# Kernel optimization log

Hardware: AMD Instinct MI355X
Metric: run time of the kernel (lower is better)

## Reference

```python
import jax, jax.numpy as jnp
import numpy as np

N_EMBD = 768
N_HEAD = 12
HEAD_DIM = N_EMBD // N_HEAD  # 64


def setup_inputs() -> dict:
    key = jax.random.key(0)
    k1, k2, k3 = jax.random.split(key, 3)
    B, S = 4, 2048
    x = jax.random.normal(k1, (B, S, N_EMBD), dtype=jnp.float32)
    W_attn = jax.random.normal(k2, (N_EMBD, 3 * N_EMBD), dtype=jnp.float32) * 0.02
    b_attn = jax.random.normal(k3, (3 * N_EMBD,), dtype=jnp.float32) * 0.02
    return {"x": x, "W_attn": W_attn, "b_attn": b_attn}


def reference(x, W_attn, b_attn):
    B, S, E = x.shape
    H, D = N_HEAD, HEAD_DIM
    # fused QKV projection (torch Linear: x @ W^T + b; here W_attn stored as [E, 3E])
    qkv = x @ W_attn + b_attn  # [B, S, 3E]
    q, k, v = jnp.split(qkv, 3, axis=-1)
    q = q.reshape(B, S, H, D)
    k = k.reshape(B, S, H, D)
    v = v.reshape(B, S, H, D)
    scale = 1.0 / np.sqrt(D).astype(np.float32)
    scores = jnp.einsum('bqhd,bkhd->bhqk', q, k) * scale  # [B, H, S, S]
    causal = jnp.tril(jnp.ones((S, S), dtype=bool))
    # ReLU attention nonlinearity (no softmax); masked entries -> 0
    att = jnp.where(causal, jnp.maximum(scores, 0.0), 0.0)
    y = jnp.einsum('bhqk,bkhd->bqhd', att, v)  # [B, S, H, D]
    return y.reshape(B, S, E)
```

## Files before the change

### kernel.cpp

```cpp
#include <hip/hip_runtime.h>

typedef __attribute__((ext_vector_type(8))) short short8;
typedef __attribute__((ext_vector_type(4))) short short4v;
typedef __attribute__((ext_vector_type(4))) float floatx4;
typedef __attribute__((ext_vector_type(2))) unsigned int uint2v;

#define S_LEN 2048
#define NH 12
#define HD 64
#define EMB 768
#define E3 2304
#define N_ITEMS 768

__device__ __forceinline__ unsigned short f2bf(float f) {
    unsigned int u = __builtin_bit_cast(unsigned int, f);
    u += 0x7FFFu + ((u >> 16) & 1u);
    return (unsigned short)(u >> 16);
}

__device__ __forceinline__ unsigned int pack2bf(float a, float b) {
#if __has_builtin(__builtin_amdgcn_cvt_pk_bf16_f32)
    typedef __attribute__((ext_vector_type(2))) short short2v;
    short2v r = __builtin_amdgcn_cvt_pk_bf16_f32(a, b);
    return __builtin_bit_cast(unsigned int, r);
#else
    return (unsigned int)f2bf(a) | ((unsigned int)f2bf(b) << 16);
#endif
}

__device__ __forceinline__ void gl_lds16(const void* g, void* l) {
    __builtin_amdgcn_global_load_lds(
        (const __attribute__((address_space(1))) unsigned int*)g,
        (__attribute__((address_space(3))) unsigned int*)l, 16, 0, 0);
}

__global__ __launch_bounds__(256) void conv_fused(const float* __restrict__ x,
                                                  ushort* __restrict__ xb,
                                                  const float* __restrict__ W,
                                                  ushort* __restrict__ Wt,
                                                  int* __restrict__ counter) {
    int tid = threadIdx.x;
    if (blockIdx.x == 0 && tid == 0) *counter = 0;
    if (blockIdx.x < 6144) {
        int i = (blockIdx.x * 256 + tid) * 4;
        float4 f = *(const float4*)(x + i);
        ushort4 o;
        o.x = f2bf(f.x); o.y = f2bf(f.y); o.z = f2bf(f.z); o.w = f2bf(f.w);
        *(ushort4*)(xb + i) = o;
    } else {
        __shared__ float tile[32][33];
        int b2 = blockIdx.x - 6144;
        int n0 = (b2 % 72) * 32, k0 = (b2 / 72) * 32;
        int tx = tid & 31, ty = tid >> 5;
        for (int i = 0; i < 4; i++)
            tile[ty + i * 8][tx] = W[(size_t)(k0 + ty + i * 8) * E3 + n0 + tx];
        __syncthreads();
        for (int i = 0; i < 4; i++)
            Wt[(size_t)(n0 + ty + i * 8) * EMB + k0 + tx] = f2bf(tile[tx][ty + i * 8]);
    }
}

__global__ __launch_bounds__(256) void qkv_gemm(const ushort* __restrict__ Xb,
                                                const ushort* __restrict__ Wt,
                                                const float* __restrict__ bias,
                                                ushort* __restrict__ QKb,
                                                ushort* __restrict__ Vt) {
    __shared__ ushort lds[33792 / 2];
    ushort* Ald = lds;
    ushort* Bld = lds + 128 * 64;
    int tid  = threadIdx.x;
    int wv = tid >> 6, lane = tid & 63;
    int l15 = lane & 15, quad = lane >> 4;
    int r8 = lane >> 3, cc = lane & 7;
    int wm = wv >> 1, wn = wv & 1;
    int m0 = blockIdx.x * 128, n0 = blockIdx.y * 128;

    floatx4 acc[4][4] = {};

    for (int k0 = 0; k0 < EMB; k0 += 64) {
        __syncthreads();
        for (int i = 0; i < 4; i++) {
            int row = wv * 32 + i * 8 + r8;
            int gc  = cc ^ r8;
            gl_lds16(Xb + (size_t)(m0 + row) * EMB + k0 + gc * 8,
                     (char*)Ald + (wv * 32 + i * 8) * 128);
            gl_lds16(Wt + (size_t)(n0 + row) * EMB + k0 + gc * 8,
                     (char*)Bld + (wv * 32 + i * 8) * 128);
        }
        __syncthreads();
        for (int ch = 0; ch < 2; ch++) {
            int sw = ((ch * 4 + quad) ^ (l15 & 7)) * 16;
            short8 af[4], bf[4];
            for (int mi = 0; mi < 4; mi++)
                af[mi] = *(const short8*)((const char*)Ald + (wm * 64 + mi * 16 + l15) * 128 + sw);
            for (int ni = 0; ni < 4; ni++)
                bf[ni] = *(const short8*)((const char*)Bld + (wn * 64 + ni * 16 + l15) * 128 + sw);
            for (int mi = 0; mi < 4; mi++)
                for (int ni = 0; ni < 4; ni++)
                    acc[mi][ni] = __builtin_amdgcn_mfma_f32_16x16x32_bf16(
                        af[mi], bf[ni], acc[mi][ni], 0, 0, 0);
        }
    }

    __syncthreads();
    if (n0 < 1536) {
        float scale = (n0 < 768) ? 0.125f : 1.0f;
        for (int ni = 0; ni < 4; ni++) {
            int nl = wn * 64 + ni * 16 + l15;
            float bv = bias[n0 + nl];
            for (int mi = 0; mi < 4; mi++)
                for (int r = 0; r < 4; r++) {
                    int ml = wm * 64 + mi * 16 + quad * 4 + r;
                    lds[ml * 132 + nl] = f2bf((acc[mi][ni][r] + bv) * scale);
                }
        }
        __syncthreads();
        int row = tid >> 1, half = tid & 1;
        size_t gm = (size_t)(m0 + row);
        for (int i = 0; i < 8; i++) {
            uint4 v = *(const uint4*)&lds[row * 132 + half * 64 + i * 8];
            *(uint4*)&QKb[gm * 1536 + n0 + half * 64 + i * 8] = v;
        }
    } else {
        for (int ni = 0; ni < 4; ni++) {
            int nl = wn * 64 + ni * 16 + l15;
            float bv = bias[n0 + nl];
            for (int mi = 0; mi < 4; mi++) {
                int ml = wm * 64 + mi * 16 + quad * 4;
                ushort4 pk4;
                pk4.x = f2bf(acc[mi][ni][0] + bv);
                pk4.y = f2bf(acc[mi][ni][1] + bv);
                pk4.z = f2bf(acc[mi][ni][2] + bv);
                pk4.w = f2bf(acc[mi][ni][3] + bv);
                *(ushort4*)&lds[nl * 132 + ml] = pk4;
            }
        }
        __syncthreads();
        int row = tid >> 1, half = tid & 1;
        int nn = n0 + row - 1536;
        int h = nn >> 6, d = nn & 63;
        int b = m0 >> 11, s0 = m0 & 2047;
        for (int i = 0; i < 8; i++) {
            uint4 v = *(const uint4*)&lds[row * 132 + half * 64 + i * 8];
            *(uint4*)&Vt[((size_t)(b * NH + h) * 64 + d) * S_LEN + s0 + half * 64 + i * 8] = v;
        }
    }
}

__global__ __launch_bounds__(256) void attn(const ushort* __restrict__ QKb,
                                            const ushort* __restrict__ Vt,
                                            float* __restrict__ out,
                                            int* __restrict__ counter) {
    __shared__ ushort Kld[2][128 * 64];
    __shared__ ushort Vld[2][64 * 128];
    int* slot = (int*)&Kld[0][0];
    int tid = threadIdx.x;
    int w = tid >> 6, lane = tid & 63;
    int l15 = lane & 15, quad = lane >> 4;
    int r8 = lane >> 3, cc = lane & 7;

    while (true) {
        __syncthreads();
        if (tid == 0) *slot = atomicAdd(counter, 1);
        __syncthreads();
        int it = *slot;
        __syncthreads();
        if (it >= N_ITEMS) break;
        int qt = 15 - it / 48;
        int bh = it % 48;
        int bg = bh / NH, h = bh % NH;

        const ushort* Qcol = QKb + (size_t)bg * S_LEN * 1536 + h * 64;
        const ushort* Kcol = QKb + (size_t)bg * S_LEN * 1536 + 768 + h * 64;
        const ushort* Vbase = Vt + (size_t)bh * HD * S_LEN;

        short8 qf[2][2];
        for (int nq = 0; nq < 2; nq++)
            for (int ch = 0; ch < 2; ch++)
                qf[nq][ch] = *(const short8*)(Qcol +
                    (size_t)(qt * 128 + w * 32 + nq * 16 + l15) * 1536 + ch * 32 + quad * 8);

        floatx4 acco[2][4] = {};
        int nst = qt + 1;

        {
            for (int i = 0; i < 4; i++) {
                int rK = w * 32 + i * 8;
                gl_lds16(Kcol + (size_t)(rK + r8) * 1536 + (cc ^ r8) * 8,
                         (char*)Kld[0] + rK * 128);
            }
            for (int i = 0; i < 4; i++) {
                int rV = w * 16 + i * 4;
                int rr = lane >> 4;
                int gc = (lane & 15) ^ ((i * 4 + rr) & 15);
                gl_lds16(Vbase + (size_t)(rV + rr) * S_LEN + gc * 8,
                         (char*)Vld[0] + rV * 256);
            }
        }

        int p = 0;
        for (int st_i = 0; st_i < nst; st_i++) {
            __syncthreads();
            if (st_i + 1 < nst) {
                const ushort* Kc = Kcol + (size_t)(st_i + 1) * 128 * 1536;
                const ushort* Vc = Vbase + (size_t)(st_i + 1) * 128;
                for (int i = 0; i < 4; i++) {
                    int rK = w * 32 + i * 8;
                    gl_lds16(Kc + (size_t)(rK + r8) * 1536 + (cc ^ r8) * 8,
                             (char*)Kld[p ^ 1] + rK * 128);
                }
                for (int i = 0; i < 4; i++) {
                    int rV = w * 16 + i * 4;
                    int rr = lane >> 4;
                    int gc = (lane & 15) ^ ((i * 4 + rr) & 15);
                    gl_lds16(Vc + (size_t)(rV + rr) * S_LEN + gc * 8,
                             (char*)Vld[p ^ 1] + rV * 256);
                }
            }
            bool diag = (st_i == qt);

            for (int jsub = 0; jsub < 2; jsub++) {
                floatx4 st[4][2] = {};
                for (int ch = 0; ch < 2; ch++) {
                    int sw = ((ch * 4 + quad) ^ (l15 & 7)) * 16;
                    short8 kf[4];
                    for (int mk = 0; mk < 4; mk++)
                        kf[mk] = *(const short8*)((const char*)Kld[p] +
                                  (jsub * 64 + mk * 16 + l15) * 128 + sw);
                    for (int mk = 0; mk < 4; mk++)
                        for (int nq = 0; nq < 2; nq++)
                            st[mk][nq] = __builtin_amdgcn_mfma_f32_16x16x32_bf16(
                                kf[mk], qf[nq][ch], st[mk][nq], 0, 0, 0);
                }

                unsigned int pk[4][2][2];
                for (int mk = 0; mk < 4; mk++) {
                    for (int nq = 0; nq < 2; nq++) {
                        float e[4];
                        for (int r = 0; r < 4; r++)
                            e[r] = fmaxf(st[mk][nq][r], 0.0f);
                        if (diag) {
                            int kg = (st_i * 2 + jsub) * 64 + mk * 16 + quad * 4;
                            int qg = qt * 128 + w * 32 + nq * 16 + l15;
                            for (int r = 0; r < 4; r++)
                                if (kg + r > qg) e[r] = 0.0f;
                        }
                        pk[mk][nq][0] = pack2bf(e[0], e[1]);
                        pk[mk][nq][1] = pack2bf(e[2], e[3]);
                    }
                }

                for (int mk = 0; mk < 4; mk++) {
                    int u = jsub * 8 + mk * 2 + (quad >> 1);
                    short4v vf[4];
                    for (int ni = 0; ni < 4; ni++)
                        vf[ni] = *(const short4v*)((const char*)Vld[p] +
                                  (ni * 16 + l15) * 256 + (u ^ l15) * 16 + (quad & 1) * 8);
                    for (int mi = 0; mi < 2; mi++) {
                        short4v a = __builtin_bit_cast(short4v,
                                     (uint2v){pk[mk][mi][0], pk[mk][mi][1]});
                        for (int ni = 0; ni < 4; ni++)
                            acco[mi][ni] = __builtin_amdgcn_mfma_f32_16x16x16bf16_1k(
                                a, vf[ni], acco[mi][ni], 0, 0, 0);
                    }
                }
            }
            p ^= 1;
        }

        for (int mi = 0; mi < 2; mi++) {
            for (int ni = 0; ni < 4; ni++) {
                int d = ni * 16 + l15;
                for (int r = 0; r < 4; r++) {
                    int s = qt * 128 + w * 32 + mi * 16 + quad * 4 + r;
                    out[((size_t)bg * S_LEN + s) * EMB + h * 64 + d] = acco[mi][ni][r];
                }
            }
        }
    }
}

extern "C" void kernel_launch(void* const* d_in, const int* in_sizes, int n_in,
                              void* d_out, int out_size, void* d_ws, size_t ws_size,
                              hipStream_t stream) {
    const float* x    = (const float*)d_in[0];
    const float* W    = (const float*)d_in[1];
    const float* bias = (const float*)d_in[2];
    float* out = (float*)d_out;

    char* ws = (char*)d_ws;
    const size_t SZ_X  = (size_t)8192 * EMB * 2;
    const size_t SZ_W  = (size_t)E3 * EMB * 2;
    const size_t SZ_QK = (size_t)8192 * 1536 * 2;
    const size_t SZ_V  = (size_t)48 * HD * S_LEN * 2;
    ushort* Xb  = (ushort*)(ws);
    ushort* Wt  = (ushort*)(ws + SZ_X);
    ushort* QKb = (ushort*)(ws + SZ_X + SZ_W);
    ushort* Vt  = (ushort*)(ws + SZ_X + SZ_W + SZ_QK);
    int* counter = (int*)(ws + SZ_X + SZ_W + SZ_QK + SZ_V);

    conv_fused<<<dim3(6144 + 1728), dim3(256), 0, stream>>>(x, Xb, W, Wt, counter);
    qkv_gemm<<<dim3(64, 18), dim3(256), 0, stream>>>(Xb, Wt, bias, QKb, Vt);
    attn<<<dim3(512), dim3(256), 0, stream>>>(QKb, Vt, out, counter);
}
```

Baseline: 187.6 us.

## Widen QKV GEMM tiles and replace atomic scheduler with static paired work assignment

```diff
diff --git a/kernel.cpp b/kernel.cpp
--- a/kernel.cpp
+++ b/kernel.cpp
@@ -10,7 +10,6 @@
 #define HD 64
 #define EMB 768
 #define E3 2304
-#define N_ITEMS 768
 
 __device__ __forceinline__ unsigned short f2bf(float f) {
     unsigned int u = __builtin_bit_cast(unsigned int, f);
@@ -37,10 +36,8 @@
 __global__ __launch_bounds__(256) void conv_fused(const float* __restrict__ x,
                                                   ushort* __restrict__ xb,
                                                   const float* __restrict__ W,
-                                                  ushort* __restrict__ Wt,
-                                                  int* __restrict__ counter) {
+                                                  ushort* __restrict__ Wt) {
     int tid = threadIdx.x;
-    if (blockIdx.x == 0 && tid == 0) *counter = 0;
     if (blockIdx.x < 6144) {
         int i = (blockIdx.x * 256 + tid) * 4;
         float4 f = *(const float4*)(x + i);
@@ -65,115 +62,161 @@
                                                 const float* __restrict__ bias,
                                                 ushort* __restrict__ QKb,
                                                 ushort* __restrict__ Vt) {
-    __shared__ ushort lds[33792 / 2];
-    ushort* Ald = lds;
-    ushort* Bld = lds + 128 * 64;
+    __shared__ ushort lds[24576];
+    char* ldsb = (char*)lds;
     int tid  = threadIdx.x;
     int wv = tid >> 6, lane = tid & 63;
     int l15 = lane & 15, quad = lane >> 4;
     int r8 = lane >> 3, cc = lane & 7;
     int wm = wv >> 1, wn = wv & 1;
-    int m0 = blockIdx.x * 128, n0 = blockIdx.y * 128;
-
-    floatx4 acc[4][4] = {};
-
-    for (int k0 = 0; k0 < EMB; k0 += 64) {
+    int m0 = blockIdx.x * 128, n0 = blockIdx.y * 256;
+
+    floatx4 acc[4][8] = {};
+
+    const char* ag = (const char*)(Xb + (size_t)m0 * EMB)
+                   + (wv * 32 + r8) * 1536 + (cc ^ r8) * 16;
+    const char* bgp = (const char*)(Wt + (size_t)n0 * EMB)
+                   + (wv * 64 + r8) * 1536 + (cc ^ r8) * 16;
+    int ast = (wv * 32) * 128;
+    int bst = 16384 + (wv * 64) * 128;
+    int afo[2], bfo[2];
+    for (int ch = 0; ch < 2; ch++) {
+        int sw = ((ch * 4 + quad) ^ (l15 & 7)) * 16;
+        afo[ch] = wm * 8192 + l15 * 128 + sw;
+        bfo[ch] = 16384 + wn * 16384 + l15 * 128 + sw;
+    }
+
+    for (int k0 = 0; k0 < 12; k0++) {
         __syncthreads();
-        for (int i = 0; i < 4; i++) {
-            int row = wv * 32 + i * 8 + r8;
-            int gc  = cc ^ r8;
-            gl_lds16(Xb + (size_t)(m0 + row) * EMB + k0 + gc * 8,
-                     (char*)Ald + (wv * 32 + i * 8) * 128);
-            gl_lds16(Wt + (size_t)(n0 + row) * EMB + k0 + gc * 8,
-                     (char*)Bld + (wv * 32 + i * 8) * 128);
-        }
+        for (int i = 0; i < 4; i++)
+            gl_lds16(ag + i * 12288, ldsb + ast + i * 1024);
+        for (int i = 0; i < 8; i++)
+            gl_lds16(bgp + i * 12288, ldsb + bst + i * 1024);
+        ag += 128;  bgp += 128;
         __syncthreads();
         for (int ch = 0; ch < 2; ch++) {
-            int sw = ((ch * 4 + quad) ^ (l15 & 7)) * 16;
-            short8 af[4], bf[4];
+            short8 af[4], bf[8];
             for (int mi = 0; mi < 4; mi++)
-                af[mi] = *(const short8*)((const char*)Ald + (wm * 64 + mi * 16 + l15) * 128 + sw);
-            for (int ni = 0; ni < 4; ni++)
-                bf[ni] = *(const short8*)((const char*)Bld + (wn * 64 + ni * 16 + l15) * 128 + sw);
+                af[mi] = *(const short8*)(ldsb + afo[ch] + mi * 2048);
+            for (int ni = 0; ni < 8; ni++)
+                bf[ni] = *(const short8*)(ldsb + bfo[ch] + ni * 2048);
             for (int mi = 0; mi < 4; mi++)
-                for (int ni = 0; ni < 4; ni++)
+                for (int ni = 0; ni < 8; ni++)
                     acc[mi][ni] = __builtin_amdgcn_mfma_f32_16x16x32_bf16(
                         af[mi], bf[ni], acc[mi][ni], 0, 0, 0);
         }
     }
 
     __syncthreads();
-    if (n0 < 1536) {
-        float scale = (n0 < 768) ? 0.125f : 1.0f;
-        for (int ni = 0; ni < 4; ni++) {
-            int nl = wn * 64 + ni * 16 + l15;
-            float bv = bias[n0 + nl];
-            for (int mi = 0; mi < 4; mi++)
-                for (int r = 0; r < 4; r++) {
-                    int ml = wm * 64 + mi * 16 + quad * 4 + r;
-                    lds[ml * 132 + nl] = f2bf((acc[mi][ni][r] + bv) * scale);
-                }
-        }
-        __syncthreads();
-        int row = tid >> 1, half = tid & 1;
-        size_t gm = (size_t)(m0 + row);
-        for (int i = 0; i < 8; i++) {
-            uint4 v = *(const uint4*)&lds[row * 132 + half * 64 + i * 8];
-            *(uint4*)&QKb[gm * 1536 + n0 + half * 64 + i * 8] = v;
+    int seg = n0 / EMB;
+    if (seg < 2) {
+        float scale = (seg == 0) ? 0.125f : 1.0f;
+        for (int h = 0; h < 2; h++) {
+            if (wn == h) {
+                for (int ni = 0; ni < 8; ni++) {
+                    int nl = ni * 16 + l15;
+                    float bv = bias[n0 + h * 128 + nl];
+                    for (int mi = 0; mi < 4; mi++)
+                        for (int r = 0; r < 4; r++) {
+                            int ml = wm * 64 + mi * 16 + quad * 4 + r;
+                            lds[ml * 136 + nl] = f2bf((acc[mi][ni][r] + bv) * scale);
+                        }
+                }
+            }
+            __syncthreads();
+            int row = tid >> 1, half2 = tid & 1;
+            size_t gm = (size_t)(m0 + row);
+            for (int i = 0; i < 8; i++) {
+                uint4 v = *(const uint4*)&lds[row * 136 + half2 * 64 + i * 8];
+                *(uint4*)&QKb[gm * 1536 + n0 + h * 128 + half2 * 64 + i * 8] = v;
+            }
+            __syncthreads();
         }
     } else {
-        for (int ni = 0; ni < 4; ni++) {
-            int nl = wn * 64 + ni * 16 + l15;
-            float bv = bias[n0 + nl];
-            for (int mi = 0; mi < 4; mi++) {
-                int ml = wm * 64 + mi * 16 + quad * 4;
-                ushort4 pk4;
-                pk4.x = f2bf(acc[mi][ni][0] + bv);
-                pk4.y = f2bf(acc[mi][ni][1] + bv);
-                pk4.z = f2bf(acc[mi][ni][2] + bv);
-                pk4.w = f2bf(acc[mi][ni][3] + bv);
-                *(ushort4*)&lds[nl * 132 + ml] = pk4;
-            }
-        }
-        __syncthreads();
-        int row = tid >> 1, half = tid & 1;
-        int nn = n0 + row - 1536;
-        int h = nn >> 6, d = nn & 63;
-        int b = m0 >> 11, s0 = m0 & 2047;
-        for (int i = 0; i < 8; i++) {
-            uint4 v = *(const uint4*)&lds[row * 132 + half * 64 + i * 8];
-            *(uint4*)&Vt[((size_t)(b * NH + h) * 64 + d) * S_LEN + s0 + half * 64 + i * 8] = v;
+        for (int h = 0; h < 2; h++) {
+            if (wn == h) {
+                for (int ni = 0; ni < 8; ni++) {
+                    int nl = ni * 16 + l15;
+                    float bv = bias[n0 + h * 128 + nl];
+                    for (int mi = 0; mi < 4; mi++) {
+                        int ml = wm * 64 + mi * 16 + quad * 4;
+                        ushort4 p4;
+                        p4.x = f2bf(acc[mi][ni][0] + bv);
+                        p4.y = f2bf(acc[mi][ni][1] + bv);
+                        p4.z = f2bf(acc[mi][ni][2] + bv);
+                        p4.w = f2bf(acc[mi][ni][3] + bv);
+                        *(ushort4*)&lds[nl * 136 + ml] = p4;
+                    }
+                }
+            }
+            __syncthreads();
+            int row = tid >> 1, half2 = tid & 1;
+            int nn = n0 + h * 128 + row - 1536;
+            int hh = nn >> 6, d = nn & 63;
+            int bb = m0 >> 11, s0 = m0 & 2047;
+            for (int i = 0; i < 8; i++) {
+                uint4 v = *(const uint4*)&lds[row * 136 + half2 * 64 + i * 8];
+                *(uint4*)&Vt[((size_t)(bb * NH + hh) * HD + d) * S_LEN + s0 + half2 * 64 + i * 8] = v;
+            }
+            __syncthreads();
         }
     }
 }
 
 __global__ __launch_bounds__(256) void attn(const ushort* __restrict__ QKb,
                                             const ushort* __restrict__ Vt,
-                                            float* __restrict__ out,
-                                            int* __restrict__ counter) {
-    __shared__ ushort Kld[2][128 * 64];
-    __shared__ ushort Vld[2][64 * 128];
-    int* slot = (int*)&Kld[0][0];
+                                            float* __restrict__ out) {
+    __shared__ ushort lds[32768];
+    char* ldsb = (char*)lds;
     int tid = threadIdx.x;
     int w = tid >> 6, lane = tid & 63;
     int l15 = lane & 15, quad = lane >> 4;
     int r8 = lane >> 3, cc = lane & 7;
-
-    while (true) {
-        __syncthreads();
-        if (tid == 0) *slot = atomicAdd(counter, 1);
-        __syncthreads();
-        int it = *slot;
-        __syncthreads();
-        if (it >= N_ITEMS) break;
-        int qt = 15 - it / 48;
-        int bh = it % 48;
-        int bg = bh / NH, h = bh % NH;
-
+    int qh = quad >> 1, qlo = quad & 1;
+    int rr = lane >> 4;
+
+    int kfo[2];
+    for (int ch = 0; ch < 2; ch++)
+        kfo[ch] = l15 * 128 + ((ch * 4 + quad) ^ (l15 & 7)) * 16;
+    int vfo[8];
+    for (int t = 0; t < 8; t++)
+        vfo[t] = 32768 + l15 * 256 + qlo * 8 + ((2 * t + qh) ^ l15) * 16;
+    int rhs[2] = { w * 32 + l15, w * 32 + 16 + l15 };
+    int kgo = (w * 32 + r8) * 3072 + (cc ^ r8) * 16;
+    int vgo[4];
+    for (int i = 0; i < 4; i++)
+        vgo[i] = (w * 16 + i * 4 + rr) * 4096 + (((lane & 15) ^ ((i * 4 + rr) & 15)) * 16);
+    int kst = (w * 32) * 128;
+    int vst = 32768 + (w * 16) * 256;
+
+    int b = blockIdx.x;
+    int nit, qts[2], bhs[2];
+    if (b < 240)      { nit = 1; qts[0] = 15 - b / 48; bhs[0] = b % 48; qts[1] = 0; bhs[1] = 0; }
+    else if (b < 480) { int j = b - 240; nit = 2; qts[0] = 10 - j / 48; bhs[0] = j % 48;
+                        qts[1] = 1 + j / 48; bhs[1] = j % 48; }
+    else              { int j = b - 480; nit = 2; qts[0] = 0; bhs[0] = 2 * j;
+                        qts[1] = 0; bhs[1] = 2 * j + 1; }
+
+    const char* kg[2]; const char* vg[2];
+    for (int i = 0; i < 2; i++) {
+        int bh = bhs[i], bg = bh / NH, h = bh % NH;
+        kg[i] = (const char*)(QKb + (size_t)bg * S_LEN * 1536 + 768 + h * 64) + kgo;
+        vg[i] = (const char*)(Vt + (size_t)bh * HD * S_LEN);
+    }
+
+    auto prefetch = [&](const char* kbase, const char* vbase, int dstP) {
+        for (int i = 0; i < 4; i++)
+            gl_lds16(kbase + i * 24576, ldsb + dstP * 16384 + kst + i * 1024);
+        for (int i = 0; i < 4; i++)
+            gl_lds16(vbase + vgo[i], ldsb + dstP * 16384 + vst + i * 1024);
+    };
+
+    int p = 0;
+    prefetch(kg[0], vg[0], 0);
+    for (int ii = 0; ii < nit; ii++) {
+        int qt = qts[ii];
+        int bh = bhs[ii], bg = bh / NH, h = bh % NH;
         const ushort* Qcol = QKb + (size_t)bg * S_LEN * 1536 + h * 64;
-        const ushort* Kcol = QKb + (size_t)bg * S_LEN * 1536 + 768 + h * 64;
-        const ushort* Vbase = Vt + (size_t)bh * HD * S_LEN;
-
         short8 qf[2][2];
         for (int nq = 0; nq < 2; nq++)
             for (int ch = 0; ch < 2; ch++)
@@ -182,55 +225,26 @@
 
         floatx4 acco[2][4] = {};
         int nst = qt + 1;
-
-        {
-            for (int i = 0; i < 4; i++) {
-                int rK = w * 32 + i * 8;
-                gl_lds16(Kcol + (size_t)(rK + r8) * 1536 + (cc ^ r8) * 8,
-                         (char*)Kld[0] + rK * 128);
-            }
-            for (int i = 0; i < 4; i++) {
-                int rV = w * 16 + i * 4;
-                int rr = lane >> 4;
-                int gc = (lane & 15) ^ ((i * 4 + rr) & 15);
-                gl_lds16(Vbase + (size_t)(rV + rr) * S_LEN + gc * 8,
-                         (char*)Vld[0] + rV * 256);
-            }
-        }
-
-        int p = 0;
-        for (int st_i = 0; st_i < nst; st_i++) {
-            __syncthreads();
-            if (st_i + 1 < nst) {
-                const ushort* Kc = Kcol + (size_t)(st_i + 1) * 128 * 1536;
-                const ushort* Vc = Vbase + (size_t)(st_i + 1) * 128;
-                for (int i = 0; i < 4; i++) {
-                    int rK = w * 32 + i * 8;
-                    gl_lds16(Kc + (size_t)(rK + r8) * 1536 + (cc ^ r8) * 8,
-                             (char*)Kld[p ^ 1] + rK * 128);
-                }
-                for (int i = 0; i < 4; i++) {
-                    int rV = w * 16 + i * 4;
-                    int rr = lane >> 4;
-                    int gc = (lane & 15) ^ ((i * 4 + rr) & 15);
-                    gl_lds16(Vc + (size_t)(rV + rr) * S_LEN + gc * 8,
-                             (char*)Vld[p ^ 1] + rV * 256);
-                }
-            }
-            bool diag = (st_i == qt);
+        for (int st = 0; st < nst; st++) {
+            __syncthreads();
+            if (st + 1 < nst)
+                prefetch(kg[ii] + (size_t)(st + 1) * 393216, vg[ii] + (st + 1) * 256, p ^ 1);
+            else if (ii + 1 < nit)
+                prefetch(kg[ii + 1], vg[ii + 1], p ^ 1);
+
+            bool diag = (st == qt);
+            const char* kb = ldsb + p * 16384;
 
             for (int jsub = 0; jsub < 2; jsub++) {
-                floatx4 st[4][2] = {};
+                floatx4 stc[4][2] = {};
                 for (int ch = 0; ch < 2; ch++) {
-                    int sw = ((ch * 4 + quad) ^ (l15 & 7)) * 16;
                     short8 kf[4];
                     for (int mk = 0; mk < 4; mk++)
-                        kf[mk] = *(const short8*)((const char*)Kld[p] +
-                                  (jsub * 64 + mk * 16 + l15) * 128 + sw);
+                        kf[mk] = *(const short8*)(kb + kfo[ch] + jsub * 8192 + mk * 2048);
                     for (int mk = 0; mk < 4; mk++)
                         for (int nq = 0; nq < 2; nq++)
-                            st[mk][nq] = __builtin_amdgcn_mfma_f32_16x16x32_bf16(
-                                kf[mk], qf[nq][ch], st[mk][nq], 0, 0, 0);
+                            stc[mk][nq] = __builtin_amdgcn_mfma_f32_16x16x32_bf16(
+                                kf[mk], qf[nq][ch], stc[mk][nq], 0, 0, 0);
                 }
 
                 unsigned int pk[4][2][2];
@@ -238,12 +252,11 @@
                     for (int nq = 0; nq < 2; nq++) {
                         float e[4];
                         for (int r = 0; r < 4; r++)
-                            e[r] = fmaxf(st[mk][nq][r], 0.0f);
+                            e[r] = fmaxf(stc[mk][nq][r], 0.0f);
                         if (diag) {
-                            int kg = (st_i * 2 + jsub) * 64 + mk * 16 + quad * 4;
-                            int qg = qt * 128 + w * 32 + nq * 16 + l15;
+                            int kl = jsub * 64 + mk * 16 + quad * 4;
                             for (int r = 0; r < 4; r++)
-                                if (kg + r > qg) e[r] = 0.0f;
+                                if (kl + r > rhs[nq]) e[r] = 0.0f;
                         }
                         pk[mk][nq][0] = pack2bf(e[0], e[1]);
                         pk[mk][nq][1] = pack2bf(e[2], e[3]);
@@ -251,11 +264,10 @@
                 }
 
                 for (int mk = 0; mk < 4; mk++) {
-                    int u = jsub * 8 + mk * 2 + (quad >> 1);
+                    int t = jsub * 4 + mk;
                     short4v vf[4];
                     for (int ni = 0; ni < 4; ni++)
-                        vf[ni] = *(const short4v*)((const char*)Vld[p] +
-                                  (ni * 16 + l15) * 256 + (u ^ l15) * 16 + (quad & 1) * 8);
+                        vf[ni] = *(const short4v*)(kb + vfo[t] + ni * 4096);
                     for (int mi = 0; mi < 2; mi++) {
                         short4v a = __builtin_bit_cast(short4v,
                                      (uint2v){pk[mk][mi][0], pk[mk][mi][1]});
@@ -292,14 +304,12 @@
     const size_t SZ_X  = (size_t)8192 * EMB * 2;
     const size_t SZ_W  = (size_t)E3 * EMB * 2;
     const size_t SZ_QK = (size_t)8192 * 1536 * 2;
-    const size_t SZ_V  = (size_t)48 * HD * S_LEN * 2;
     ushort* Xb  = (ushort*)(ws);
     ushort* Wt  = (ushort*)(ws + SZ_X);
     ushort* QKb = (ushort*)(ws + SZ_X + SZ_W);
     ushort* Vt  = (ushort*)(ws + SZ_X + SZ_W + SZ_QK);
-    int* counter = (int*)(ws + SZ_X + SZ_W + SZ_QK + SZ_V);
-
-    conv_fused<<<dim3(6144 + 1728), dim3(256), 0, stream>>>(x, Xb, W, Wt, counter);
-    qkv_gemm<<<dim3(64, 18), dim3(256), 0, stream>>>(Xb, Wt, bias, QKb, Vt);
-    attn<<<dim3(512), dim3(256), 0, stream>>>(QKb, Vt, out, counter);
-}
+
+    conv_fused<<<dim3(6144 + 1728), dim3(256), 0, stream>>>(x, Xb, W, Wt);
+    qkv_gemm<<<dim3(64, 9), dim3(256), 0, stream>>>(Xb, Wt, bias, QKb, Vt);
+    attn<<<dim3(504), dim3(256), 0, stream>>>(QKb, Vt, out);
+}
```

New measurement: 216.6 us. +15.5%, slower.
